# Performance work log

Hardware: AMD Instinct MI355X
Metric: run time of the kernel (lower is better)

Reference implementation:

```python
import jax, jax.numpy as jnp
import numpy as np

B, S, C, NH = 4, 2048, 1024, 16
HD = C // NH


def setup_inputs() -> dict:
    key = jax.random.key(0)
    ks = jax.random.split(key, 8)
    w = lambda k, shape: (jax.random.normal(k, shape, dtype=jnp.float32) * 0.02)
    return {
        "x": jax.random.normal(ks[0], (B, S, C), dtype=jnp.float32),
        "y": jax.random.normal(ks[1], (B, S, C), dtype=jnp.float32),
        "mask": jnp.zeros((B, S), dtype=bool),  # True = padded key
        "Wq_w": w(ks[2], (C, C)),
        "Wq_b": jnp.zeros((C,), dtype=jnp.float32),
        "Wkv_w": w(ks[3], (2 * C, C)),
        "Wkv_b": jnp.zeros((2 * C,), dtype=jnp.float32),
        "Wo_w": w(ks[4], (C, C)),
        "Wo_b": jnp.zeros((C,), dtype=jnp.float32),
    }


def reference(x, y, mask, Wq_w, Wq_b, Wkv_w, Wkv_b, Wo_w, Wo_b):
    b, s, c = x.shape
    # projections (torch nn.Linear: x @ W.T + b)
    q = (x @ Wq_w.T + Wq_b).reshape(b, s, NH, HD).transpose(0, 2, 1, 3)  # bhsd
    kv = (y @ Wkv_w.T + Wkv_b).reshape(b, s, 2, NH, HD)
    k = kv[:, :, 0].transpose(0, 2, 1, 3)  # bhsd
    v = kv[:, :, 1].transpose(0, 2, 1, 3)  # bhsd
    # scores: [b, h, s_q, s_k]
    attn = jnp.einsum("bhqd,bhkd->bhqk", q, k) / np.sqrt(HD).astype(np.float32)
    causal = jnp.triu(jnp.ones((s, s), dtype=bool), 1)  # True above diagonal
    combined = causal[None, None] | mask[:, None, None, :]
    attn = jnp.where(combined, -jnp.inf, attn)
    attn = jax.nn.softmax(attn, axis=-1)
    out = jnp.einsum("bhqk,bhkd->bhqd", attn, v)
    out = out.transpose(0, 2, 1, 3).reshape(b, s, c)
    return out @ Wo_w.T + Wo_b
```

## Files before the change

kernel.cpp:

```cpp
#include <hip/hip_runtime.h>
#include <stdint.h>

#define B_  4
#define S_  2048
#define C_  1024
#define NH_ 16
#define HD_ 64
#define M_  (B_*S_)
#define NT_ (S_/64)

typedef __attribute__((ext_vector_type(8))) short bf16x8;
typedef __attribute__((ext_vector_type(4))) float f32x4;

typedef __attribute__((address_space(1))) const unsigned int gu32;
typedef __attribute__((address_space(3))) unsigned int lu32;

__device__ __forceinline__ void gload16(const void* g, void* l) {
    __builtin_amdgcn_global_load_lds((gu32*)g, (lu32*)l, 16, 0, 0);
}

__device__ __forceinline__ unsigned short f2bf(float f) {
    union { float f; unsigned u; } v; v.f = f;
    unsigned r = v.u + 0x7FFF + ((v.u >> 16) & 1);
    return (unsigned short)(r >> 16);
}

__global__ __launch_bounds__(256)
void cvt_all(const float4* __restrict__ x, const float4* __restrict__ y,
             const float4* __restrict__ wq, const float4* __restrict__ wkv,
             const float4* __restrict__ wo,
             uint4* __restrict__ xb, uint4* __restrict__ yb, uint4* __restrict__ wqb,
             uint4* __restrict__ wkvb, uint4* __restrict__ wob) {
    int i = blockIdx.x * 256 + threadIdx.x;
    const float4* src; uint4* dst; int off;
    if      (i < 1048576) { src = x;   dst = xb;   off = i; }
    else if (i < 2097152) { src = y;   dst = yb;   off = i - 1048576; }
    else if (i < 2228224) { src = wq;  dst = wqb;  off = i - 2097152; }
    else if (i < 2490368) { src = wkv; dst = wkvb; off = i - 2228224; }
    else                  { src = wo;  dst = wob;  off = i - 2490368; }
    float4 a = src[2*off], b = src[2*off+1];
    union { unsigned short s[8]; uint4 v; } u;
    u.s[0]=f2bf(a.x); u.s[1]=f2bf(a.y); u.s[2]=f2bf(a.z); u.s[3]=f2bf(a.w);
    u.s[4]=f2bf(b.x); u.s[5]=f2bf(b.y); u.s[6]=f2bf(b.z); u.s[7]=f2bf(b.w);
    dst[off] = u.v;
}

__global__ __launch_bounds__(64)
void mask_bits(const unsigned char* __restrict__ mp, unsigned long long* __restrict__ mw) {
    int b = blockIdx.x, lane = threadIdx.x;
    for (int w = 0; w < NT_; ++w) {
        unsigned long long bal = __ballot(mp[b*S_ + w*64 + lane] != 0);
        if (lane == 0) mw[b*NT_ + w] = bal;
    }
}

#define BM 128
#define BN 128
#define BK 64

__global__ __launch_bounds__(256)
void gemm_bt(const unsigned short* __restrict__ A, const unsigned short* __restrict__ Bt,
             const float* __restrict__ bias,
             unsigned short* __restrict__ out0, unsigned short* __restrict__ out1,
             float* __restrict__ outf, int K, int N, int mode)
{
    __shared__ unsigned short As[BM*BK];
    __shared__ unsigned short Bs[BN*BK];
    int t = threadIdx.x;
    int lane = t & 63, w = t >> 6;
    int wx = w & 1, wy = w >> 1;
    int quad = lane >> 4, l16 = lane & 15;
    int bx = blockIdx.x, by = blockIdx.y;

    f32x4 acc[4][4] = {};
    int rowA = by * BM, rowB = bx * BN;
    int lr = lane >> 3;
    int lc = (lane & 7) * 8;
    const unsigned short* gA = A  + (size_t)(rowA + w*32 + lr)*K + lc;
    const unsigned short* gB = Bt + (size_t)(rowB + w*32 + lr)*K + lc;
    unsigned short* lA = &As[(w*32)*BK];
    unsigned short* lB = &Bs[(w*32)*BK];

    for (int kb = 0; kb < K; kb += BK) {
        #pragma unroll
        for (int i = 0; i < 4; ++i) {
            gload16(gA + (size_t)i*8*K + kb, lA + i*8*BK);
            gload16(gB + (size_t)i*8*K + kb, lB + i*8*BK);
        }
        asm volatile("s_waitcnt vmcnt(0)" ::: "memory");
        __syncthreads();
        #pragma unroll
        for (int ks = 0; ks < 2; ++ks) {
            bf16x8 af[4], bfr[4];
            #pragma unroll
            for (int mt = 0; mt < 4; ++mt)
                af[mt] = *reinterpret_cast<const bf16x8*>(&As[(wy*64 + mt*16 + l16)*BK + ks*32 + quad*8]);
            #pragma unroll
            for (int nt = 0; nt < 4; ++nt)
                bfr[nt] = *reinterpret_cast<const bf16x8*>(&Bs[(wx*64 + nt*16 + l16)*BK + ks*32 + quad*8]);
            #pragma unroll
            for (int mt = 0; mt < 4; ++mt)
                #pragma unroll
                for (int nt = 0; nt < 4; ++nt)
                    acc[mt][nt] = __builtin_amdgcn_mfma_f32_16x16x32_bf16(af[mt], bfr[nt], acc[mt][nt], 0, 0, 0);
        }
        __syncthreads();
    }

    const float QSCALE = 0.180336880111f;
    #pragma unroll
    for (int mt = 0; mt < 4; ++mt) {
        #pragma unroll
        for (int nt = 0; nt < 4; ++nt) {
            int gn = bx*BN + wx*64 + nt*16 + l16;
            float bv = bias[gn];
            #pragma unroll
            for (int r = 0; r < 4; ++r) {
                int gm = by*BM + wy*64 + mt*16 + quad*4 + r;
                float v = acc[mt][nt][r] + bv;
                if (mode == 2) {
                    outf[(size_t)gm * N + gn] = v;
                } else if (mode == 0) {
                    v *= QSCALE;
                    int b = gm >> 11, s = gm & 2047;
                    int h = gn >> 6,  d = gn & 63;
                    out0[(((size_t)(b*NH_ + h)*S_ + s) << 6) + d] = f2bf(v);
                } else {
                    int b = gm >> 11, s = gm & 2047;
                    if (gn < C_) {
                        int h = gn >> 6, d = gn & 63;
                        out0[(((size_t)(b*NH_ + h)*S_ + s) << 6) + d] = f2bf(v);
                    } else {
                        int n2 = gn - C_;
                        int h = n2 >> 6, d = n2 & 63;
                        out1[((size_t)(b*NH_ + h)*HD_ + d)*S_ + s] = f2bf(v);
                    }
                }
            }
        }
    }
}

__global__ __launch_bounds__(256, 4)
void attn_kernel(const unsigned short* __restrict__ Qg, const unsigned short* __restrict__ Kg,
                 const unsigned short* __restrict__ Vt, const unsigned long long* __restrict__ mw,
                 unsigned short* __restrict__ att)
{
    __shared__ unsigned short Pl[64*72];
    __shared__ float Lbuf[4][64];
    __shared__ float Linv[64];
    int t = threadIdx.x, lane = t & 63, w = t >> 6;
    int quad = lane >> 4, l16 = lane & 15;
    int bh = blockIdx.x, b = bh >> 4, h = bh & 15;
    int qi = blockIdx.y;

    const unsigned short* kbase = Kg + ((size_t)bh*S_ + w*16 + l16)*HD_ + quad*8;
    const unsigned short* vbase = Vt + ((size_t)bh*HD_ + w*16 + l16)*S_ + quad*8;
    int kp_row = w*16 + quad*4;

    for (int half = 0; half < 2; ++half) {
        int qt = half ? (NT_ - 1 - qi) : qi;

        bf16x8 qf[4][2];
        #pragma unroll
        for (int m = 0; m < 4; ++m) {
            const unsigned short* qp = Qg + ((size_t)bh*S_ + qt*64 + m*16 + l16)*HD_;
            qf[m][0] = *reinterpret_cast<const bf16x8*>(qp + quad*8);
            qf[m][1] = *reinterpret_cast<const bf16x8*>(qp + 32 + quad*8);
        }
        f32x4 oacc[4] = {};
        float lsum[4] = {0.f, 0.f, 0.f, 0.f};

        bf16x8 kc0 = *reinterpret_cast<const bf16x8*>(kbase);
        bf16x8 kc1 = *reinterpret_cast<const bf16x8*>(kbase + 32);

        for (int kt = 0; kt <= qt; ++kt) {
            int ktn = (kt < qt) ? kt + 1 : kt;
            const unsigned short* kpn = kbase + (size_t)ktn*64*HD_;
            bf16x8 kn0 = *reinterpret_cast<const bf16x8*>(kpn);
            bf16x8 kn1 = *reinterpret_cast<const bf16x8*>(kpn + 32);
            const unsigned short* vp = vbase + kt*64;
            bf16x8 vc0 = *reinterpret_cast<const bf16x8*>(vp);
            bf16x8 vc1 = *reinterpret_cast<const bf16x8*>(vp + 32);

            f32x4 sacc[4];
            #pragma unroll
            for (int m = 0; m < 4; ++m) {
                sacc[m] = __builtin_amdgcn_mfma_f32_16x16x32_bf16(kc0, qf[m][0], f32x4{}, 0, 0, 0);
                sacc[m] = __builtin_amdgcn_mfma_f32_16x16x32_bf16(kc1, qf[m][1], sacc[m], 0, 0, 0);
            }

            unsigned long long mword = mw[b*NT_ + kt];
            unsigned nib = (unsigned)(mword >> (w*16 + quad*4)) & 0xFu;
            float padd[4];
            #pragma unroll
            for (int r = 0; r < 4; ++r) padd[r] = ((nib >> r) & 1u) ? -1e30f : 0.f;
            bool diag = (kt == qt);

            #pragma unroll
            for (int m = 0; m < 4; ++m) {
                float p[4];
                #pragma unroll
                for (int r = 0; r < 4; ++r) {
                    float s = sacc[m][r] + padd[r];
                    if (diag && (kp_row + r > m*16 + l16)) s = -1e30f;
                    p[r] = exp2f(s);
                }
                lsum[m] += (p[0] + p[1]) + (p[2] + p[3]);
                unsigned lo = (__float_as_uint(p[0]) >> 16) | (__float_as_uint(p[1]) & 0xFFFF0000u);
                unsigned hi = (__float_as_uint(p[2]) >> 16) | (__float_as_uint(p[3]) & 0xFFFF0000u);
                *reinterpret_cast<uint2*>(&Pl[(m*16 + l16)*72 + w*16 + quad*4]) = make_uint2(lo, hi);
            }
            __syncthreads();
            #pragma unroll
            for (int m = 0; m < 4; ++m) {
                bf16x8 pf0 = *reinterpret_cast<const bf16x8*>(&Pl[(m*16 + l16)*72 + quad*8]);
                bf16x8 pf1 = *reinterpret_cast<const bf16x8*>(&Pl[(m*16 + l16)*72 + 32 + quad*8]);
                oacc[m] = __builtin_amdgcn_mfma_f32_16x16x32_bf16(pf0, vc0, oacc[m], 0, 0, 0);
                oacc[m] = __builtin_amdgcn_mfma_f32_16x16x32_bf16(pf1, vc1, oacc[m], 0, 0, 0);
            }
            __syncthreads();
            kc0 = kn0; kc1 = kn1;
        }

        #pragma unroll
        for (int m = 0; m < 4; ++m) {
            lsum[m] += __shfl_xor(lsum[m], 16, 64);
            lsum[m] += __shfl_xor(lsum[m], 32, 64);
            Lbuf[w][m*16 + l16] = lsum[m];
        }
        __syncthreads();
        int q64 = t & 63;
        Linv[q64] = 1.0f / (Lbuf[0][q64] + Lbuf[1][q64] + Lbuf[2][q64] + Lbuf[3][q64]);
        __syncthreads();
        #pragma unroll
        for (int m = 0; m < 4; ++m) {
            #pragma unroll
            for (int r = 0; r < 4; ++r) {
                float iv = Linv[m*16 + quad*4 + r];
                int q = qt*64 + m*16 + quad*4 + r;
                att[((size_t)(b*S_ + q))*C_ + h*HD_ + w*16 + l16] = f2bf(oacc[m][r] * iv);
            }
        }
        __syncthreads();
    }
}

extern "C" void kernel_launch(void* const* d_in, const int* in_sizes, int n_in,
                              void* d_out, int out_size, void* d_ws, size_t ws_size,
                              hipStream_t stream) {
    const float* x     = (const float*)d_in[0];
    const float* y     = (const float*)d_in[1];
    const unsigned char* mask = (const unsigned char*)d_in[2];
    const float* Wq_w  = (const float*)d_in[3];
    const float* Wq_b  = (const float*)d_in[4];
    const float* Wkv_w = (const float*)d_in[5];
    const float* Wkv_b = (const float*)d_in[6];
    const float* Wo_w  = (const float*)d_in[7];
    const float* Wo_b  = (const float*)d_in[8];
    float* out = (float*)d_out;

    unsigned short* xb   = (unsigned short*)d_ws;
    unsigned short* yb   = xb   + (size_t)M_*C_;
    unsigned short* Wqb  = yb   + (size_t)M_*C_;
    unsigned short* Wkvb = Wqb  + (size_t)C_*C_;
    unsigned short* Wob  = Wkvb + (size_t)2*C_*C_;
    unsigned short* Qg   = Wob  + (size_t)C_*C_;
    unsigned short* Kg   = Qg   + (size_t)M_*C_;
    unsigned short* Vtg  = Kg   + (size_t)M_*C_;
    unsigned long long* maskw = (unsigned long long*)yb;
    unsigned short* att  = xb;

    cvt_all<<<10240, 256, 0, stream>>>((const float4*)x, (const float4*)y,
        (const float4*)Wq_w, (const float4*)Wkv_w, (const float4*)Wo_w,
        (uint4*)xb, (uint4*)yb, (uint4*)Wqb, (uint4*)Wkvb, (uint4*)Wob);

    gemm_bt<<<dim3(C_/BN, M_/BM), 256, 0, stream>>>(xb, Wqb, Wq_b, Qg, nullptr, nullptr, C_, C_, 0);
    gemm_bt<<<dim3(2*C_/BN, M_/BM), 256, 0, stream>>>(yb, Wkvb, Wkv_b, Kg, Vtg, nullptr, C_, 2*C_, 1);
    mask_bits<<<B_, 64, 0, stream>>>(mask, maskw);
    attn_kernel<<<dim3(B_*NH_, NT_/2), 256, 0, stream>>>(Qg, Kg, Vtg, maskw, att);
    gemm_bt<<<dim3(C_/BN, M_/BM), 256, 0, stream>>>(att, Wob, Wo_b, nullptr, nullptr, out, C_, C_, 2);
}
```

Before: 354.6 us.

## Keep P in registers for PV MFMA, split key dim across waves, reduce in LDS

The attention PV step no longer stages P through shared memory with two barriers per key tile. Each wave keeps its 16-key slice of P in registers as a half-zero-padded bf16 MFMA operand and accumulates a full 64x64 partial output. The four partial outputs are reduced through LDS at the end. The change also skips fully masked diagonal sub-blocks, uses the raw exp2 builtin, templates the GEMM mode, and lowers the occupancy hint to 3. It removes the per-tile barriers and LDS traffic, but wastes half of every PV MFMA on zero padding, quadruples the accumulator registers, and adds an epilogue reduction.

```diff
diff --git a/kernel.cpp b/kernel.cpp
--- a/kernel.cpp
+++ b/kernel.cpp
@@ -58,11 +58,12 @@
 #define BN 128
 #define BK 64
 
+template<int MODE>
 __global__ __launch_bounds__(256)
 void gemm_bt(const unsigned short* __restrict__ A, const unsigned short* __restrict__ Bt,
              const float* __restrict__ bias,
              unsigned short* __restrict__ out0, unsigned short* __restrict__ out1,
-             float* __restrict__ outf, int K, int N, int mode)
+             float* __restrict__ outf, int K, int N)
 {
     __shared__ unsigned short As[BM*BK];
     __shared__ unsigned short Bs[BN*BK];
@@ -118,9 +119,9 @@
             for (int r = 0; r < 4; ++r) {
                 int gm = by*BM + wy*64 + mt*16 + quad*4 + r;
                 float v = acc[mt][nt][r] + bv;
-                if (mode == 2) {
+                if (MODE == 2) {
                     outf[(size_t)gm * N + gn] = v;
-                } else if (mode == 0) {
+                } else if (MODE == 0) {
                     v *= QSCALE;
                     int b = gm >> 11, s = gm & 2047;
                     int h = gn >> 6,  d = gn & 63;
@@ -141,12 +142,12 @@
     }
 }
 
-__global__ __launch_bounds__(256, 4)
+__global__ __launch_bounds__(256, 3)
 void attn_kernel(const unsigned short* __restrict__ Qg, const unsigned short* __restrict__ Kg,
                  const unsigned short* __restrict__ Vt, const unsigned long long* __restrict__ mw,
                  unsigned short* __restrict__ att)
 {
-    __shared__ unsigned short Pl[64*72];
+    __shared__ float Obuf[2][64*66];
     __shared__ float Lbuf[4][64];
     __shared__ float Linv[64];
     int t = threadIdx.x, lane = t & 63, w = t >> 6;
@@ -155,8 +156,7 @@
     int qi = blockIdx.y;
 
     const unsigned short* kbase = Kg + ((size_t)bh*S_ + w*16 + l16)*HD_ + quad*8;
-    const unsigned short* vbase = Vt + ((size_t)bh*HD_ + w*16 + l16)*S_ + quad*8;
-    int kp_row = w*16 + quad*4;
+    const unsigned short* vbase = Vt + ((size_t)bh*HD_ + l16)*S_ + w*16 + quad*4;
 
     for (int half = 0; half < 2; ++half) {
         int qt = half ? (NT_ - 1 - qi) : qi;
@@ -168,7 +168,7 @@
             qf[m][0] = *reinterpret_cast<const bf16x8*>(qp + quad*8);
             qf[m][1] = *reinterpret_cast<const bf16x8*>(qp + 32 + quad*8);
         }
-        f32x4 oacc[4] = {};
+        f32x4 oacc[4][4] = {};
         float lsum[4] = {0.f, 0.f, 0.f, 0.f};
 
         bf16x8 kc0 = *reinterpret_cast<const bf16x8*>(kbase);
@@ -179,9 +179,16 @@
             const unsigned short* kpn = kbase + (size_t)ktn*64*HD_;
             bf16x8 kn0 = *reinterpret_cast<const bf16x8*>(kpn);
             bf16x8 kn1 = *reinterpret_cast<const bf16x8*>(kpn + 32);
+
+            bf16x8 vB[4];
             const unsigned short* vp = vbase + kt*64;
-            bf16x8 vc0 = *reinterpret_cast<const bf16x8*>(vp);
-            bf16x8 vc1 = *reinterpret_cast<const bf16x8*>(vp + 32);
+            #pragma unroll
+            for (int nt = 0; nt < 4; ++nt) {
+                uint2 raw = *reinterpret_cast<const uint2*>(vp + (size_t)nt*16*S_);
+                union { unsigned u[4]; bf16x8 v; } vb;
+                vb.u[0] = raw.x; vb.u[1] = raw.y; vb.u[2] = 0; vb.u[3] = 0;
+                vB[nt] = vb.v;
+            }
 
             f32x4 sacc[4];
             #pragma unroll
@@ -199,27 +206,23 @@
 
             #pragma unroll
             for (int m = 0; m < 4; ++m) {
+                if (diag && w > m) continue;
                 float p[4];
                 #pragma unroll
                 for (int r = 0; r < 4; ++r) {
                     float s = sacc[m][r] + padd[r];
-                    if (diag && (kp_row + r > m*16 + l16)) s = -1e30f;
-                    p[r] = exp2f(s);
+                    if (diag && w == m && (quad*4 + r > l16)) s = -1e30f;
+                    p[r] = __builtin_amdgcn_exp2f(s);
                 }
                 lsum[m] += (p[0] + p[1]) + (p[2] + p[3]);
-                unsigned lo = (__float_as_uint(p[0]) >> 16) | (__float_as_uint(p[1]) & 0xFFFF0000u);
-                unsigned hi = (__float_as_uint(p[2]) >> 16) | (__float_as_uint(p[3]) & 0xFFFF0000u);
-                *reinterpret_cast<uint2*>(&Pl[(m*16 + l16)*72 + w*16 + quad*4]) = make_uint2(lo, hi);
-            }
-            __syncthreads();
-            #pragma unroll
-            for (int m = 0; m < 4; ++m) {
-                bf16x8 pf0 = *reinterpret_cast<const bf16x8*>(&Pl[(m*16 + l16)*72 + quad*8]);
-                bf16x8 pf1 = *reinterpret_cast<const bf16x8*>(&Pl[(m*16 + l16)*72 + 32 + quad*8]);
-                oacc[m] = __builtin_amdgcn_mfma_f32_16x16x32_bf16(pf0, vc0, oacc[m], 0, 0, 0);
-                oacc[m] = __builtin_amdgcn_mfma_f32_16x16x32_bf16(pf1, vc1, oacc[m], 0, 0, 0);
-            }
-            __syncthreads();
+                unsigned pk01 = __builtin_amdgcn_perm(__float_as_uint(p[1]), __float_as_uint(p[0]), 0x07060302u);
+                unsigned pk23 = __builtin_amdgcn_perm(__float_as_uint(p[3]), __float_as_uint(p[2]), 0x07060302u);
+                union { unsigned u[4]; bf16x8 v; } pa;
+                pa.u[0] = pk01; pa.u[1] = pk23; pa.u[2] = 0; pa.u[3] = 0;
+                #pragma unroll
+                for (int nt = 0; nt < 4; ++nt)
+                    oacc[m][nt] = __builtin_amdgcn_mfma_f32_16x16x32_bf16(pa.v, vB[nt], oacc[m][nt], 0, 0, 0);
+            }
             kc0 = kn0; kc1 = kn1;
         }
 
@@ -229,17 +232,36 @@
             lsum[m] += __shfl_xor(lsum[m], 32, 64);
             Lbuf[w][m*16 + l16] = lsum[m];
         }
-        __syncthreads();
+        if (w < 2) {
+            #pragma unroll
+            for (int m = 0; m < 4; ++m)
+                #pragma unroll
+                for (int nt = 0; nt < 4; ++nt)
+                    #pragma unroll
+                    for (int r = 0; r < 4; ++r)
+                        Obuf[w][(m*16 + quad*4 + r)*66 + nt*16 + l16] = oacc[m][nt][r];
+        }
+        __syncthreads();
+        if (w >= 2) {
+            float* ob = Obuf[w - 2];
+            #pragma unroll
+            for (int m = 0; m < 4; ++m)
+                #pragma unroll
+                for (int nt = 0; nt < 4; ++nt)
+                    #pragma unroll
+                    for (int r = 0; r < 4; ++r)
+                        ob[(m*16 + quad*4 + r)*66 + nt*16 + l16] += oacc[m][nt][r];
+        }
         int q64 = t & 63;
         Linv[q64] = 1.0f / (Lbuf[0][q64] + Lbuf[1][q64] + Lbuf[2][q64] + Lbuf[3][q64]);
         __syncthreads();
         #pragma unroll
-        for (int m = 0; m < 4; ++m) {
+        for (int nt = 0; nt < 4; ++nt) {
             #pragma unroll
             for (int r = 0; r < 4; ++r) {
-                float iv = Linv[m*16 + quad*4 + r];
-                int q = qt*64 + m*16 + quad*4 + r;
-                att[((size_t)(b*S_ + q))*C_ + h*HD_ + w*16 + l16] = f2bf(oacc[m][r] * iv);
+                int row = w*16 + quad*4 + r;
+                float v = Obuf[0][row*66 + nt*16 + l16] + Obuf[1][row*66 + nt*16 + l16];
+                att[((size_t)(b*S_ + qt*64 + row))*C_ + h*HD_ + nt*16 + l16] = f2bf(v * Linv[row]);
             }
         }
         __syncthreads();
@@ -275,9 +297,9 @@
         (const float4*)Wq_w, (const float4*)Wkv_w, (const float4*)Wo_w,
         (uint4*)xb, (uint4*)yb, (uint4*)Wqb, (uint4*)Wkvb, (uint4*)Wob);
 
-    gemm_bt<<<dim3(C_/BN, M_/BM), 256, 0, stream>>>(xb, Wqb, Wq_b, Qg, nullptr, nullptr, C_, C_, 0);
-    gemm_bt<<<dim3(2*C_/BN, M_/BM), 256, 0, stream>>>(yb, Wkvb, Wkv_b, Kg, Vtg, nullptr, C_, 2*C_, 1);
+    gemm_bt<0><<<dim3(C_/BN, M_/BM), 256, 0, stream>>>(xb, Wqb, Wq_b, Qg, nullptr, nullptr, C_, C_);
+    gemm_bt<1><<<dim3(2*C_/BN, M_/BM), 256, 0, stream>>>(yb, Wkvb, Wkv_b, Kg, Vtg, nullptr, C_, 2*C_);
     mask_bits<<<B_, 64, 0, stream>>>(mask, maskw);
     attn_kernel<<<dim3(B_*NH_, NT_/2), 256, 0, stream>>>(Qg, Kg, Vtg, maskw, att);
-    gemm_bt<<<dim3(C_/BN, M_/BM), 256, 0, stream>>>(att, Wob, Wo_b, nullptr, nullptr, out, C_, C_, 2);
-}
+    gemm_bt<2><<<dim3(C_/BN, M_/BM), 256, 0, stream>>>(att, Wob, Wo_b, nullptr, nullptr, out, C_, C_);
+}
```

Result: slower. 398.8 us (+12.5%).

## Process two key tiles per sync in attention and templatize GEMM epilogue mode

Applied to the files above, without the earlier changes.

The attention inner loop now handles two 64-key tiles per iteration, writing a 64x128 P tile to shared memory so each pair of barriers covers twice the work. An odd tail tile is handled separately with the causal diagonal mask. It also uses the hardware exp2 intrinsic and byte-permute packing for bf16, and drops the cross-iteration K register prefetch. The occupancy hint drops from 4 to 3 waves to allow more registers, and the GEMM epilogue mode becomes a template parameter so the branches compile away. The trade-offs are larger shared memory and register use, and no K prefetch overlap between iterations.

```diff
diff --git a/kernel.cpp b/kernel.cpp
--- a/kernel.cpp
+++ b/kernel.cpp
@@ -58,11 +58,12 @@
 #define BN 128
 #define BK 64
 
+template<int MODE>
 __global__ __launch_bounds__(256)
 void gemm_bt(const unsigned short* __restrict__ A, const unsigned short* __restrict__ Bt,
              const float* __restrict__ bias,
              unsigned short* __restrict__ out0, unsigned short* __restrict__ out1,
-             float* __restrict__ outf, int K, int N, int mode)
+             float* __restrict__ outf, int K, int N)
 {
     __shared__ unsigned short As[BM*BK];
     __shared__ unsigned short Bs[BN*BK];
@@ -118,9 +119,9 @@
             for (int r = 0; r < 4; ++r) {
                 int gm = by*BM + wy*64 + mt*16 + quad*4 + r;
                 float v = acc[mt][nt][r] + bv;
-                if (mode == 2) {
+                if (MODE == 2) {
                     outf[(size_t)gm * N + gn] = v;
-                } else if (mode == 0) {
+                } else if (MODE == 0) {
                     v *= QSCALE;
                     int b = gm >> 11, s = gm & 2047;
                     int h = gn >> 6,  d = gn & 63;
@@ -141,12 +142,13 @@
     }
 }
 
-__global__ __launch_bounds__(256, 4)
+#define PLD 136
+__global__ __launch_bounds__(256, 3)
 void attn_kernel(const unsigned short* __restrict__ Qg, const unsigned short* __restrict__ Kg,
                  const unsigned short* __restrict__ Vt, const unsigned long long* __restrict__ mw,
                  unsigned short* __restrict__ att)
 {
-    __shared__ unsigned short Pl[64*72];
+    __shared__ unsigned short Pl[64*PLD];
     __shared__ float Lbuf[4][64];
     __shared__ float Linv[64];
     int t = threadIdx.x, lane = t & 63, w = t >> 6;
@@ -171,56 +173,115 @@
         f32x4 oacc[4] = {};
         float lsum[4] = {0.f, 0.f, 0.f, 0.f};
 
-        bf16x8 kc0 = *reinterpret_cast<const bf16x8*>(kbase);
-        bf16x8 kc1 = *reinterpret_cast<const bf16x8*>(kbase + 32);
-
-        for (int kt = 0; kt <= qt; ++kt) {
-            int ktn = (kt < qt) ? kt + 1 : kt;
-            const unsigned short* kpn = kbase + (size_t)ktn*64*HD_;
-            bf16x8 kn0 = *reinterpret_cast<const bf16x8*>(kpn);
-            bf16x8 kn1 = *reinterpret_cast<const bf16x8*>(kpn + 32);
+        int npairs = (qt + 1) >> 1;
+        bool tail = ((qt + 1) & 1) != 0;
+
+        for (int p2 = 0; p2 < npairs; ++p2) {
+            int ktA = 2*p2, ktB = 2*p2 + 1;
+            bool diagB = (!tail && p2 == npairs - 1);
+
+            const unsigned short* kpA = kbase + (size_t)ktA*64*HD_;
+            const unsigned short* kpB = kbase + (size_t)ktB*64*HD_;
+            bf16x8 kA0 = *reinterpret_cast<const bf16x8*>(kpA);
+            bf16x8 kA1 = *reinterpret_cast<const bf16x8*>(kpA + 32);
+            bf16x8 kB0 = *reinterpret_cast<const bf16x8*>(kpB);
+            bf16x8 kB1 = *reinterpret_cast<const bf16x8*>(kpB + 32);
+            const unsigned short* vpA = vbase + ktA*64;
+            const unsigned short* vpB = vbase + ktB*64;
+            bf16x8 vA0 = *reinterpret_cast<const bf16x8*>(vpA);
+            bf16x8 vA1 = *reinterpret_cast<const bf16x8*>(vpA + 32);
+            bf16x8 vB0 = *reinterpret_cast<const bf16x8*>(vpB);
+            bf16x8 vB1 = *reinterpret_cast<const bf16x8*>(vpB + 32);
+
+            unsigned nibA = (unsigned)(mw[b*NT_ + ktA] >> (w*16 + quad*4)) & 0xFu;
+            unsigned nibB = (unsigned)(mw[b*NT_ + ktB] >> (w*16 + quad*4)) & 0xFu;
+            float paddA[4], paddB[4];
+            #pragma unroll
+            for (int r = 0; r < 4; ++r) {
+                paddA[r] = ((nibA >> r) & 1u) ? -1e30f : 0.f;
+                paddB[r] = ((nibB >> r) & 1u) ? -1e30f : 0.f;
+            }
+
+            #pragma unroll
+            for (int m = 0; m < 4; ++m) {
+                f32x4 sa = __builtin_amdgcn_mfma_f32_16x16x32_bf16(kA0, qf[m][0], f32x4{}, 0, 0, 0);
+                sa = __builtin_amdgcn_mfma_f32_16x16x32_bf16(kA1, qf[m][1], sa, 0, 0, 0);
+                float pA[4];
+                #pragma unroll
+                for (int r = 0; r < 4; ++r) pA[r] = __builtin_amdgcn_exp2f(sa[r] + paddA[r]);
+                lsum[m] += (pA[0] + pA[1]) + (pA[2] + pA[3]);
+                unsigned a01 = __builtin_amdgcn_perm(__float_as_uint(pA[1]), __float_as_uint(pA[0]), 0x07060302u);
+                unsigned a23 = __builtin_amdgcn_perm(__float_as_uint(pA[3]), __float_as_uint(pA[2]), 0x07060302u);
+                *reinterpret_cast<uint2*>(&Pl[(m*16 + l16)*PLD + w*16 + quad*4]) = make_uint2(a01, a23);
+                f32x4 sb = __builtin_amdgcn_mfma_f32_16x16x32_bf16(kB0, qf[m][0], f32x4{}, 0, 0, 0);
+                sb = __builtin_amdgcn_mfma_f32_16x16x32_bf16(kB1, qf[m][1], sb, 0, 0, 0);
+                float pB[4];
+                #pragma unroll
+                for (int r = 0; r < 4; ++r) {
+                    float s = sb[r] + paddB[r];
+                    if (diagB && (kp_row + r > m*16 + l16)) s = -1e30f;
+                    pB[r] = __builtin_amdgcn_exp2f(s);
+                }
+                lsum[m] += (pB[0] + pB[1]) + (pB[2] + pB[3]);
+                unsigned b01 = __builtin_amdgcn_perm(__float_as_uint(pB[1]), __float_as_uint(pB[0]), 0x07060302u);
+                unsigned b23 = __builtin_amdgcn_perm(__float_as_uint(pB[3]), __float_as_uint(pB[2]), 0x07060302u);
+                *reinterpret_cast<uint2*>(&Pl[(m*16 + l16)*PLD + 64 + w*16 + quad*4]) = make_uint2(b01, b23);
+            }
+            __syncthreads();
+            #pragma unroll
+            for (int m = 0; m < 4; ++m) {
+                const unsigned short* prow = &Pl[(m*16 + l16)*PLD + quad*8];
+                bf16x8 pf0 = *reinterpret_cast<const bf16x8*>(prow);
+                bf16x8 pf1 = *reinterpret_cast<const bf16x8*>(prow + 32);
+                bf16x8 pf2 = *reinterpret_cast<const bf16x8*>(prow + 64);
+                bf16x8 pf3 = *reinterpret_cast<const bf16x8*>(prow + 96);
+                oacc[m] = __builtin_amdgcn_mfma_f32_16x16x32_bf16(pf0, vA0, oacc[m], 0, 0, 0);
+                oacc[m] = __builtin_amdgcn_mfma_f32_16x16x32_bf16(pf1, vA1, oacc[m], 0, 0, 0);
+                oacc[m] = __builtin_amdgcn_mfma_f32_16x16x32_bf16(pf2, vB0, oacc[m], 0, 0, 0);
+                oacc[m] = __builtin_amdgcn_mfma_f32_16x16x32_bf16(pf3, vB1, oacc[m], 0, 0, 0);
+            }
+            __syncthreads();
+        }
+
+        if (tail) {
+            int kt = qt;
+            const unsigned short* kp = kbase + (size_t)kt*64*HD_;
+            bf16x8 kc0 = *reinterpret_cast<const bf16x8*>(kp);
+            bf16x8 kc1 = *reinterpret_cast<const bf16x8*>(kp + 32);
             const unsigned short* vp = vbase + kt*64;
             bf16x8 vc0 = *reinterpret_cast<const bf16x8*>(vp);
             bf16x8 vc1 = *reinterpret_cast<const bf16x8*>(vp + 32);
-
-            f32x4 sacc[4];
+            unsigned nib = (unsigned)(mw[b*NT_ + kt] >> (w*16 + quad*4)) & 0xFu;
+            float padd[4];
+            #pragma unroll
+            for (int r = 0; r < 4; ++r) padd[r] = ((nib >> r) & 1u) ? -1e30f : 0.f;
+
             #pragma unroll
             for (int m = 0; m < 4; ++m) {
-                sacc[m] = __builtin_amdgcn_mfma_f32_16x16x32_bf16(kc0, qf[m][0], f32x4{}, 0, 0, 0);
-                sacc[m] = __builtin_amdgcn_mfma_f32_16x16x32_bf16(kc1, qf[m][1], sacc[m], 0, 0, 0);
-            }
-
-            unsigned long long mword = mw[b*NT_ + kt];
-            unsigned nib = (unsigned)(mword >> (w*16 + quad*4)) & 0xFu;
-            float padd[4];
-            #pragma unroll
-            for (int r = 0; r < 4; ++r) padd[r] = ((nib >> r) & 1u) ? -1e30f : 0.f;
-            bool diag = (kt == qt);
-
-            #pragma unroll
-            for (int m = 0; m < 4; ++m) {
+                f32x4 sa = __builtin_amdgcn_mfma_f32_16x16x32_bf16(kc0, qf[m][0], f32x4{}, 0, 0, 0);
+                sa = __builtin_amdgcn_mfma_f32_16x16x32_bf16(kc1, qf[m][1], sa, 0, 0, 0);
                 float p[4];
                 #pragma unroll
                 for (int r = 0; r < 4; ++r) {
-                    float s = sacc[m][r] + padd[r];
-                    if (diag && (kp_row + r > m*16 + l16)) s = -1e30f;
-                    p[r] = exp2f(s);
+                    float s = sa[r] + padd[r];
+                    if (kp_row + r > m*16 + l16) s = -1e30f;
+                    p[r] = __builtin_amdgcn_exp2f(s);
                 }
                 lsum[m] += (p[0] + p[1]) + (p[2] + p[3]);
-                unsigned lo = (__float_as_uint(p[0]) >> 16) | (__float_as_uint(p[1]) & 0xFFFF0000u);
-                unsigned hi = (__float_as_uint(p[2]) >> 16) | (__float_as_uint(p[3]) & 0xFFFF0000u);
-                *reinterpret_cast<uint2*>(&Pl[(m*16 + l16)*72 + w*16 + quad*4]) = make_uint2(lo, hi);
+                unsigned a01 = __builtin_amdgcn_perm(__float_as_uint(p[1]), __float_as_uint(p[0]), 0x07060302u);
+                unsigned a23 = __builtin_amdgcn_perm(__float_as_uint(p[3]), __float_as_uint(p[2]), 0x07060302u);
+                *reinterpret_cast<uint2*>(&Pl[(m*16 + l16)*PLD + w*16 + quad*4]) = make_uint2(a01, a23);
             }
             __syncthreads();
             #pragma unroll
             for (int m = 0; m < 4; ++m) {
-                bf16x8 pf0 = *reinterpret_cast<const bf16x8*>(&Pl[(m*16 + l16)*72 + quad*8]);
-                bf16x8 pf1 = *reinterpret_cast<const bf16x8*>(&Pl[(m*16 + l16)*72 + 32 + quad*8]);
+                const unsigned short* prow = &Pl[(m*16 + l16)*PLD + quad*8];
+                bf16x8 pf0 = *reinterpret_cast<const bf16x8*>(prow);
+                bf16x8 pf1 = *reinterpret_cast<const bf16x8*>(prow + 32);
                 oacc[m] = __builtin_amdgcn_mfma_f32_16x16x32_bf16(pf0, vc0, oacc[m], 0, 0, 0);
                 oacc[m] = __builtin_amdgcn_mfma_f32_16x16x32_bf16(pf1, vc1, oacc[m], 0, 0, 0);
             }
             __syncthreads();
-            kc0 = kn0; kc1 = kn1;
         }
 
         #pragma unroll
@@ -275,9 +336,9 @@
         (const float4*)Wq_w, (const float4*)Wkv_w, (const float4*)Wo_w,
         (uint4*)xb, (uint4*)yb, (uint4*)Wqb, (uint4*)Wkvb, (uint4*)Wob);
 
-    gemm_bt<<<dim3(C_/BN, M_/BM), 256, 0, stream>>>(xb, Wqb, Wq_b, Qg, nullptr, nullptr, C_, C_, 0);
-    gemm_bt<<<dim3(2*C_/BN, M_/BM), 256, 0, stream>>>(yb, Wkvb, Wkv_b, Kg, Vtg, nullptr, C_, 2*C_, 1);
+    gemm_bt<0><<<dim3(C_/BN, M_/BM), 256, 0, stream>>>(xb, Wqb, Wq_b, Qg, nullptr, nullptr, C_, C_);
+    gemm_bt<1><<<dim3(2*C_/BN, M_/BM), 256, 0, stream>>>(yb, Wkvb, Wkv_b, Kg, Vtg, nullptr, C_, 2*C_);
     mask_bits<<<B_, 64, 0, stream>>>(mask, maskw);
     attn_kernel<<<dim3(B_*NH_, NT_/2), 256, 0, stream>>>(Qg, Kg, Vtg, maskw, att);
-    gemm_bt<<<dim3(C_/BN, M_/BM), 256, 0, stream>>>(att, Wob, Wo_b, nullptr, nullptr, out, C_, C_, 2);
-}
+    gemm_bt<2><<<dim3(C_/BN, M_/BM), 256, 0, stream>>>(att, Wob, Wo_b, nullptr, nullptr, out, C_, C_);
+}
```

Result: slower. 362.1 us (+2.1%).

## Fuse Q and KV projections into one launch, read mask bytes directly in attention

Applied to the files above, without the earlier changes.

Merges the Q and KV projection GEMMs into a single launch, with MODE now a template parameter so the epilogue branch is resolved at compile time. The separate mask_bits kernel is removed; the attention kernel reads four mask bytes per row and zeroes the probabilities of padded keys. The causal-mask test now runs only on the diagonal tile, exp2 uses the hardware builtin, and bf16 packing uses v_perm. The aim is fewer launches and less per-element ALU work, at the cost of applying the padding mask after exp instead of before.

```diff
diff --git a/kernel.cpp b/kernel.cpp
--- a/kernel.cpp
+++ b/kernel.cpp
@@ -45,32 +45,22 @@
     dst[off] = u.v;
 }
 
-__global__ __launch_bounds__(64)
-void mask_bits(const unsigned char* __restrict__ mp, unsigned long long* __restrict__ mw) {
-    int b = blockIdx.x, lane = threadIdx.x;
-    for (int w = 0; w < NT_; ++w) {
-        unsigned long long bal = __ballot(mp[b*S_ + w*64 + lane] != 0);
-        if (lane == 0) mw[b*NT_ + w] = bal;
-    }
-}
-
 #define BM 128
 #define BN 128
 #define BK 64
 
-__global__ __launch_bounds__(256)
-void gemm_bt(const unsigned short* __restrict__ A, const unsigned short* __restrict__ Bt,
-             const float* __restrict__ bias,
-             unsigned short* __restrict__ out0, unsigned short* __restrict__ out1,
-             float* __restrict__ outf, int K, int N, int mode)
+template<int MODE>
+__device__ __forceinline__
+void gemm_body(const unsigned short* __restrict__ A, const unsigned short* __restrict__ Bt,
+               const float* __restrict__ bias,
+               unsigned short* __restrict__ out0, unsigned short* __restrict__ out1,
+               float* __restrict__ outf, int K, int N, int bx, int by,
+               unsigned short* As, unsigned short* Bs)
 {
-    __shared__ unsigned short As[BM*BK];
-    __shared__ unsigned short Bs[BN*BK];
     int t = threadIdx.x;
     int lane = t & 63, w = t >> 6;
     int wx = w & 1, wy = w >> 1;
     int quad = lane >> 4, l16 = lane & 15;
-    int bx = blockIdx.x, by = blockIdx.y;
 
     f32x4 acc[4][4] = {};
     int rowA = by * BM, rowB = bx * BN;
@@ -118,9 +108,9 @@
             for (int r = 0; r < 4; ++r) {
                 int gm = by*BM + wy*64 + mt*16 + quad*4 + r;
                 float v = acc[mt][nt][r] + bv;
-                if (mode == 2) {
+                if (MODE == 2) {
                     outf[(size_t)gm * N + gn] = v;
-                } else if (mode == 0) {
+                } else if (MODE == 0) {
                     v *= QSCALE;
                     int b = gm >> 11, s = gm & 2047;
                     int h = gn >> 6,  d = gn & 63;
@@ -141,9 +131,37 @@
     }
 }
 
+__global__ __launch_bounds__(256)
+void proj_fused(const unsigned short* __restrict__ xb, const unsigned short* __restrict__ Wqb,
+                const float* __restrict__ Wq_b,
+                const unsigned short* __restrict__ yb, const unsigned short* __restrict__ Wkvb,
+                const float* __restrict__ Wkv_b,
+                unsigned short* __restrict__ Qg, unsigned short* __restrict__ Kg,
+                unsigned short* __restrict__ Vt)
+{
+    __shared__ unsigned short As[BM*BK];
+    __shared__ unsigned short Bs[BN*BK];
+    int id = blockIdx.x;
+    if (id < 512) {
+        gemm_body<0>(xb, Wqb, Wq_b, Qg, nullptr, nullptr, C_, C_, id & 7, id >> 3, As, Bs);
+    } else {
+        int j = id - 512;
+        gemm_body<1>(yb, Wkvb, Wkv_b, Kg, Vt, nullptr, C_, 2*C_, j & 15, j >> 4, As, Bs);
+    }
+}
+
+__global__ __launch_bounds__(256)
+void gemm_oproj(const unsigned short* __restrict__ A, const unsigned short* __restrict__ Bt,
+                const float* __restrict__ bias, float* __restrict__ outf)
+{
+    __shared__ unsigned short As[BM*BK];
+    __shared__ unsigned short Bs[BN*BK];
+    gemm_body<2>(A, Bt, bias, nullptr, nullptr, outf, C_, C_, blockIdx.x, blockIdx.y, As, Bs);
+}
+
 __global__ __launch_bounds__(256, 4)
 void attn_kernel(const unsigned short* __restrict__ Qg, const unsigned short* __restrict__ Kg,
-                 const unsigned short* __restrict__ Vt, const unsigned long long* __restrict__ mw,
+                 const unsigned short* __restrict__ Vt, const unsigned char* __restrict__ maskp,
                  unsigned short* __restrict__ att)
 {
     __shared__ unsigned short Pl[64*72];
@@ -157,6 +175,7 @@
     const unsigned short* kbase = Kg + ((size_t)bh*S_ + w*16 + l16)*HD_ + quad*8;
     const unsigned short* vbase = Vt + ((size_t)bh*HD_ + w*16 + l16)*S_ + quad*8;
     int kp_row = w*16 + quad*4;
+    const unsigned char* mbase = maskp + (size_t)b*S_ + kp_row;
 
     for (int half = 0; half < 2; ++half) {
         int qt = half ? (NT_ - 1 - qi) : qi;
@@ -183,6 +202,8 @@
             bf16x8 vc0 = *reinterpret_cast<const bf16x8*>(vp);
             bf16x8 vc1 = *reinterpret_cast<const bf16x8*>(vp + 32);
 
+            unsigned m4 = *reinterpret_cast<const unsigned*>(mbase + kt*64);
+
             f32x4 sacc[4];
             #pragma unroll
             for (int m = 0; m < 4; ++m) {
@@ -190,26 +211,31 @@
                 sacc[m] = __builtin_amdgcn_mfma_f32_16x16x32_bf16(kc1, qf[m][1], sacc[m], 0, 0, 0);
             }
 
-            unsigned long long mword = mw[b*NT_ + kt];
-            unsigned nib = (unsigned)(mword >> (w*16 + quad*4)) & 0xFu;
-            float padd[4];
-            #pragma unroll
-            for (int r = 0; r < 4; ++r) padd[r] = ((nib >> r) & 1u) ? -1e30f : 0.f;
             bool diag = (kt == qt);
-
             #pragma unroll
             for (int m = 0; m < 4; ++m) {
                 float p[4];
-                #pragma unroll
-                for (int r = 0; r < 4; ++r) {
-                    float s = sacc[m][r] + padd[r];
-                    if (diag && (kp_row + r > m*16 + l16)) s = -1e30f;
-                    p[r] = exp2f(s);
+                if (diag) {
+                    #pragma unroll
+                    for (int r = 0; r < 4; ++r) {
+                        float s = sacc[m][r];
+                        if (kp_row + r > m*16 + l16) s = -1e30f;
+                        p[r] = __builtin_amdgcn_exp2f(s);
+                    }
+                } else {
+                    #pragma unroll
+                    for (int r = 0; r < 4; ++r)
+                        p[r] = __builtin_amdgcn_exp2f(sacc[m][r]);
+                }
+                if (m4) {
+                    #pragma unroll
+                    for (int r = 0; r < 4; ++r)
+                        if ((m4 >> (8*r)) & 0xFFu) p[r] = 0.f;
                 }
                 lsum[m] += (p[0] + p[1]) + (p[2] + p[3]);
-                unsigned lo = (__float_as_uint(p[0]) >> 16) | (__float_as_uint(p[1]) & 0xFFFF0000u);
-                unsigned hi = (__float_as_uint(p[2]) >> 16) | (__float_as_uint(p[3]) & 0xFFFF0000u);
-                *reinterpret_cast<uint2*>(&Pl[(m*16 + l16)*72 + w*16 + quad*4]) = make_uint2(lo, hi);
+                unsigned a01 = __builtin_amdgcn_perm(__float_as_uint(p[1]), __float_as_uint(p[0]), 0x07060302u);
+                unsigned a23 = __builtin_amdgcn_perm(__float_as_uint(p[3]), __float_as_uint(p[2]), 0x07060302u);
+                *reinterpret_cast<uint2*>(&Pl[(m*16 + l16)*72 + w*16 + quad*4]) = make_uint2(a01, a23);
             }
             __syncthreads();
             #pragma unroll
@@ -268,16 +294,13 @@
     unsigned short* Qg   = Wob  + (size_t)C_*C_;
     unsigned short* Kg   = Qg   + (size_t)M_*C_;
     unsigned short* Vtg  = Kg   + (size_t)M_*C_;
-    unsigned long long* maskw = (unsigned long long*)yb;
     unsigned short* att  = xb;
 
     cvt_all<<<10240, 256, 0, stream>>>((const float4*)x, (const float4*)y,
         (const float4*)Wq_w, (const float4*)Wkv_w, (const float4*)Wo_w,
         (uint4*)xb, (uint4*)yb, (uint4*)Wqb, (uint4*)Wkvb, (uint4*)Wob);
 
-    gemm_bt<<<dim3(C_/BN, M_/BM), 256, 0, stream>>>(xb, Wqb, Wq_b, Qg, nullptr, nullptr, C_, C_, 0);
-    gemm_bt<<<dim3(2*C_/BN, M_/BM), 256, 0, stream>>>(yb, Wkvb, Wkv_b, Kg, Vtg, nullptr, C_, 2*C_, 1);
-    mask_bits<<<B_, 64, 0, stream>>>(mask, maskw);
-    attn_kernel<<<dim3(B_*NH_, NT_/2), 256, 0, stream>>>(Qg, Kg, Vtg, maskw, att);
-    gemm_bt<<<dim3(C_/BN, M_/BM), 256, 0, stream>>>(att, Wob, Wo_b, nullptr, nullptr, out, C_, C_, 2);
-}
+    proj_fused<<<1536, 256, 0, stream>>>(xb, Wqb, Wq_b, yb, Wkvb, Wkv_b, Qg, Kg, Vtg);
+    attn_kernel<<<dim3(B_*NH_, NT_/2), 256, 0, stream>>>(Qg, Kg, Vtg, mask, att);
+    gemm_oproj<<<dim3(C_/BN, M_/BM), 256, 0, stream>>>(att, Wob, Wo_b, out);
+}
```

After: 328.7 us. -7.3%, faster.
